# Kernel optimization log

Hardware: AMD Instinct MI355X
Metric: run time of the kernel (lower is better)

The kernel has to match this reference:

```python
import jax, jax.numpy as jnp
from jax import lax
import numpy as np

EPS = 1e-5
K = 3


def _conv(x, w, b, pad, dil=1, groups=1):
    out = lax.conv_general_dilated(
        x, w, (1, 1), [(pad, pad), (pad, pad)], rhs_dilation=(dil, dil),
        dimension_numbers=('NCHW', 'OIHW', 'NCHW'), feature_group_count=groups)
    return out + b[None, :, None, None]


def _bn(x, g, b, m, v):
    scale = g / jnp.sqrt(v + EPS)
    return (x - m[None, :, None, None]) * scale[None, :, None, None] + b[None, :, None, None]


def setup_inputs() -> dict:
    key = jax.random.key(0)
    ks = jax.random.split(key, 24)
    B, C, H, W = 8, 256, 48, 80
    Hd = 256  # hidden_channels
    n = lambda k, s, sc=0.05: (jax.random.normal(k, s, dtype=jnp.float32) * sc)
    return {
        'f_t_minus_2': jax.random.normal(ks[0], (B, C, H, W), dtype=jnp.float32),
        'f_t_minus_1': jax.random.normal(ks[1], (B, C, H, W), dtype=jnp.float32),
        'f_t':         jax.random.normal(ks[2], (B, C, H, W), dtype=jnp.float32),
        'ov_w1': n(ks[3], (Hd, 3 * C, 3, 3)), 'ov_b1': n(ks[4], (Hd,)),
        'bn1_g': jnp.ones((Hd,), jnp.float32), 'bn1_b': jnp.zeros((Hd,), jnp.float32),
        'bn1_m': n(ks[5], (Hd,)), 'bn1_v': jax.random.uniform(ks[6], (Hd,), jnp.float32, 0.5, 1.5),
        'ov_w2': n(ks[7], (Hd, Hd, 3, 3)), 'ov_b2': n(ks[8], (Hd,)),
        'bn2_g': jnp.ones((Hd,), jnp.float32), 'bn2_b': jnp.zeros((Hd,), jnp.float32),
        'bn2_m': n(ks[9], (Hd,)), 'bn2_v': jax.random.uniform(ks[10], (Hd,), jnp.float32, 0.5, 1.5),
        'g_w': n(ks[11], (C, Hd, 1, 1)), 'g_b': n(ks[12], (C,)),
        'fc1_w': n(ks[13], (512, 2 * C)), 'fc1_b': n(ks[14], (512,)),
        'fc2_w': n(ks[15], (C * K * K, 512)), 'fc2_b': n(ks[16], (C * K * K,)),
        'ap_w': n(ks[17], (1, 2 * C, 1, 1)), 'ap_b': n(ks[18], (1,)),
        'a_w': n(ks[19], (1, 2 * C, 1, 1)), 'a_b': jnp.ones((1,), jnp.float32),
    }


def reference(f_t_minus_2, f_t_minus_1, f_t,
              ov_w1, ov_b1, bn1_g, bn1_b, bn1_m, bn1_v,
              ov_w2, ov_b2, bn2_g, bn2_b, bn2_m, bn2_v,
              g_w, g_b, fc1_w, fc1_b, fc2_w, fc2_b,
              ap_w, ap_b, a_w, a_b):
    B, C, H, W = f_t.shape
    # (1) Overview-Net (GCM)
    f_concat = jnp.concatenate([f_t_minus_2, f_t_minus_1, f_t], axis=1)
    h = jax.nn.relu(_bn(_conv(f_concat, ov_w1, ov_b1, pad=2, dil=2), bn1_g, bn1_b, bn1_m, bn1_v))
    h = jax.nn.relu(_bn(_conv(h, ov_w2, ov_b2, pad=4, dil=4), bn2_g, bn2_b, bn2_m, bn2_v))
    g_pooled = h.mean(axis=(2, 3), keepdims=True)            # [B,Hd,1,1]
    G = _conv(g_pooled, g_w, g_b, pad=0)                     # [B,C,1,1]
    # (2) Focus-Net: FC-generated per-(batch,channel) 3x3 depthwise conv on (f_t, f_{t-1})
    Fs = jnp.concatenate([f_t, f_t_minus_1], axis=0)         # [2B,C,H,W]
    g_flat = jnp.repeat(G.reshape(B, C), 2, axis=0)          # [2B,C]
    gap = Fs.mean(axis=(2, 3))                               # [2B,C]
    fc_in = jnp.concatenate([g_flat, gap], axis=1)           # [2B,2C]
    w = jax.nn.silu(fc_in @ fc1_w.T + fc1_b) @ fc2_w.T + fc2_b  # [2B, C*9]
    w = w.reshape(2 * B * C, 1, K, K)
    x = Fs.reshape(1, 2 * B * C, H, W)
    out = lax.conv_general_dilated(
        x, w, (1, 1), [(1, 1), (1, 1)],
        dimension_numbers=('NCHW', 'OIHW', 'NCHW'), feature_group_count=2 * B * C)
    out = out.reshape(2 * B, C, H, W)
    f_t_mod, f_t1_mod = out[:B], out[B:]
    # (3) Dynamic fusion
    f_prev_cat = jnp.concatenate([f_t1_mod, f_t_minus_2], axis=1)
    alpha_prev = 0.3 + 0.4 * jax.nn.sigmoid(_conv(f_prev_cat, ap_w, ap_b, pad=0))
    f_prev = alpha_prev * f_t1_mod + (1.0 - alpha_prev) * f_t_minus_2
    f_cat = jnp.concatenate([f_t_mod, f_prev], axis=1)
    alpha = 0.6 + 0.3 * jax.nn.sigmoid(_conv(f_cat, a_w, a_b, pad=0))
    return alpha * f_t_mod + (1.0 - alpha) * f_prev
```

## Files before the change

kernel.cpp:

```cpp
#include <hip/hip_runtime.h>
#include <hip/hip_bf16.h>
#include <math.h>


typedef __bf16 bf16x8 __attribute__((ext_vector_type(8)));
typedef float f32x4 __attribute__((ext_vector_type(4)));
typedef __attribute__((address_space(1))) void as1_void;
typedef __attribute__((address_space(3))) void as3_void;


__global__ __launch_bounds__(256) void prep_consts_kernel(
    const float* __restrict__ ob1, const float* __restrict__ g1, const float* __restrict__ b1,
    const float* __restrict__ m1, const float* __restrict__ v1,
    const float* __restrict__ ob2, const float* __restrict__ g2, const float* __restrict__ b2,
    const float* __restrict__ m2, const float* __restrict__ v2,
    float* __restrict__ cst)
{
  int i = threadIdx.x;
  float a1 = g1[i] / sqrtf(v1[i] + 1e-5f);
  cst[i]       = a1;
  cst[256 + i] = (ob1[i] - m1[i]) * a1 + b1[i];
  float a2 = g2[i] / sqrtf(v2[i] + 1e-5f);
  cst[512 + i] = a2;
  cst[768 + i] = (ob2[i] - m2[i]) * a2 + b2[i];
}

__global__ __launch_bounds__(256) void pad_concat_kernel(
    const float* __restrict__ f2, const float* __restrict__ f1, const float* __restrict__ f0,
    __hip_bfloat16* __restrict__ out, float* __restrict__ gapv)
{
  int bid = blockIdx.x;
  const int cg = bid % 6; bid /= 6;
  const int y = bid % 48;
  const int b = bid / 48;

  __shared__ float tile[128 * 85];

  const float* src = (cg < 2) ? f2 : ((cg < 4) ? f1 : f0);
  const int ccbase = (cg & 1) * 128;
  const uint4 z4 = {0u, 0u, 0u, 0u};

#pragma unroll
  for (int it = 0; it < 10; it++) {
    const int idx = it * 256 + threadIdx.x;
    const int cl = idx / 20, x4 = idx % 20;
    const float4 v = *(const float4*)(src +
        (((size_t)b * 256 + ccbase + cl) * 48 + y) * 80 + x4 * 4);
    float* t = tile + cl * 85 + x4 * 4;
    t[0] = v.x; t[1] = v.y; t[2] = v.z; t[3] = v.w;
  }

  if (threadIdx.x < 32) {
    const int xb_ = threadIdx.x >> 3, ch8 = threadIdx.x & 7;
    const int xx = (xb_ < 2) ? xb_ : (80 + xb_);
    *(uint4*)(out + ((size_t)(b * 52 + y + 2) * 84 + xx) * 768 + cg * 128 + ch8 * 8) = z4;
  }
  if (y == 0 || y == 47) {
    const int r0 = (y == 0) ? 0 : 50;
    for (int idx = threadIdx.x; idx < 1344; idx += 256) {
      const int rr = idx / 672, rem = idx % 672;
      const int xx = rem >> 3, ch8 = rem & 7;
      *(uint4*)(out + ((size_t)(b * 52 + r0 + rr) * 84 + xx) * 768 + cg * 128 + ch8 * 8) = z4;
    }
  }
  __syncthreads();

  __hip_bfloat16* obase = out + ((size_t)(b * 52 + y + 2) * 84 + 2) * 768 + cg * 128;
#pragma unroll
  for (int it = 0; it < 5; it++) {
    const int idx = it * 256 + threadIdx.x;
    const int chunk = idx & 15, x = idx >> 4;
    const float* t = tile + chunk * 8 * 85 + x;
    union { __hip_bfloat16 h[8]; uint4 u; } pk;
#pragma unroll
    for (int j = 0; j < 8; j++) pk.h[j] = __float2bfloat16(t[j * 85]);
    *(uint4*)(obase + (size_t)x * 768 + chunk * 8) = pk.u;
  }

  if (cg >= 2) {
    const int i_gap = (cg >= 4) ? b : (b + 8);
    const int cl = threadIdx.x >> 1, half = threadIdx.x & 1;
    const float* t = tile + cl * 85 + half * 40;
    float s = 0.f;
#pragma unroll
    for (int k = 0; k < 40; k++) s += t[k];
    s += __shfl_xor(s, 1);
    if (half == 0) atomicAdd(&gapv[i_gap * 256 + ccbase + cl], s);
  }
}

__global__ __launch_bounds__(256) void repack_w_kernel(
    const float* __restrict__ w, __hip_bfloat16* __restrict__ out, int OC, int IC)
{
  int idx = blockIdx.x * 256 + threadIdx.x;
  if (idx >= OC * IC * 9) return;
  int ic = idx % IC;
  int t = idx / IC;
  int oc = t % OC;
  int tap = t / OC;
  out[idx] = __float2bfloat16(w[(oc * IC + ic) * 9 + tap]);
}

template <int CIN, int HP, int WP, int DIL, int MODE>
__global__ __launch_bounds__(256) void conv_mfma_kernel(
    const __hip_bfloat16* __restrict__ inp, const __hip_bfloat16* __restrict__ wt,
    const float* __restrict__ bnA, const float* __restrict__ bnB,
    __hip_bfloat16* __restrict__ outp, float* __restrict__ gpool)
{
  __shared__ unsigned short As[8192] __attribute__((aligned(16)));
  __shared__ unsigned short Bs[8192] __attribute__((aligned(16)));

  int bid = blockIdx.x;
  bid = (bid & 7) * 60 + (bid >> 3);
  const int ocb = bid & 1; bid >>= 1;
  const int xb = bid % 5; bid /= 5;
  const int yb = bid % 6; bid /= 6;
  const int b = bid;
  const int y0 = yb * 8, x0 = xb * 16, oc0 = ocb * 128;

  const int t = threadIdx.x;
  const int w = t >> 6, l = t & 63;
  const int col16 = l & 15, quad = l >> 4;
  const int wm = w >> 1, wn = w & 1;
  const int rsub = l >> 3;
  const int jj = (l & 7) ^ rsub;

  f32x4 acc[4][4];
  const f32x4 zf = {0.f, 0.f, 0.f, 0.f};
#pragma unroll
  for (int i = 0; i < 4; i++)
#pragma unroll
    for (int j = 0; j < 4; j++) acc[i][j] = zf;

  for (int c0 = 0; c0 < CIN; c0 += 64) {
    for (int tap = 0; tap < 9; tap++) {
      const int ty = tap / 3, tx = tap - ty * 3;
      const __hip_bfloat16* inBase =
          inp + ((size_t)(b * HP + y0 + DIL * ty) * WP + (x0 + DIL * tx)) * CIN + jj * 8 + c0;
      const __hip_bfloat16* wBase = wt + (size_t)(tap * 256 + oc0) * CIN + jj * 8 + c0;
      __syncthreads();
#pragma unroll
      for (int i = 0; i < 4; i++) {
        const int q = i * 4 + w;
        const int m = q * 8 + rsub;
        const int ry = m >> 4, rx = m & 15;
        const __hip_bfloat16* gp = inBase + (ry * WP + rx) * CIN;
        __builtin_amdgcn_global_load_lds((as1_void*)gp,
            (as3_void*)((char*)As + q * 1024), 16, 0, 0);
      }
#pragma unroll
      for (int i = 0; i < 4; i++) {
        const int q = i * 4 + w;
        const int n = q * 8 + rsub;
        const __hip_bfloat16* gp = wBase + n * CIN;
        __builtin_amdgcn_global_load_lds((as1_void*)gp,
            (as3_void*)((char*)Bs + q * 1024), 16, 0, 0);
      }
      __syncthreads();
#pragma unroll
      for (int kiter = 0; kiter < 2; kiter++) {
        bf16x8 af[4], bg[4];
#pragma unroll
        for (int fi = 0; fi < 4; fi++) {
          const int m = wm * 64 + fi * 16 + col16;
          const int jc = (kiter * 4 + quad) ^ (m & 7);
          af[fi] = *(const bf16x8*)((const char*)As + m * 128 + jc * 16);
        }
#pragma unroll
        for (int fi = 0; fi < 4; fi++) {
          const int n = wn * 64 + fi * 16 + col16;
          const int jc = (kiter * 4 + quad) ^ (n & 7);
          bg[fi] = *(const bf16x8*)((const char*)Bs + n * 128 + jc * 16);
        }
#pragma unroll
        for (int fm_ = 0; fm_ < 4; fm_++)
#pragma unroll
          for (int fn_ = 0; fn_ < 4; fn_++)
            acc[fm_][fn_] = __builtin_amdgcn_mfma_f32_16x16x32_bf16(
                af[fm_], bg[fn_], acc[fm_][fn_], 0, 0, 0);
      }
    }
  }

  if (MODE == 0) {
#pragma unroll
    for (int fn_ = 0; fn_ < 4; fn_++) {
      const int oc = oc0 + wn * 64 + fn_ * 16 + col16;
      const float sa = bnA[oc], sb = bnB[oc];
#pragma unroll
      for (int fm_ = 0; fm_ < 4; fm_++) {
#pragma unroll
        for (int r = 0; r < 4; r++) {
          const int m = wm * 64 + fm_ * 16 + quad * 4 + r;
          const int y = y0 + (m >> 4), x = x0 + (m & 15);
          const float v = fmaxf(acc[fm_][fn_][r] * sa + sb, 0.f);
          outp[((size_t)(b * 56 + y + 4) * 88 + (x + 4)) * 256 + oc] = __float2bfloat16(v);
        }
      }
    }
  } else {
#pragma unroll
    for (int fn_ = 0; fn_ < 4; fn_++) {
      const int oc = oc0 + wn * 64 + fn_ * 16 + col16;
      const float sa = bnA[oc], sb = bnB[oc];
      float cs = 0.f;
#pragma unroll
      for (int fm_ = 0; fm_ < 4; fm_++)
#pragma unroll
        for (int r = 0; r < 4; r++)
          cs += fmaxf(acc[fm_][fn_][r] * sa + sb, 0.f);
      cs += __shfl_xor(cs, 16);
      cs += __shfl_xor(cs, 32);
      if (quad == 0) atomicAdd(&gpool[b * 256 + oc], cs);
    }
  }
}


__global__ __launch_bounds__(256) void fcG_kernel(
    const float* __restrict__ gpool, const float* __restrict__ gw,
    const float* __restrict__ gb, float* __restrict__ G)
{
  int b = blockIdx.x, oc = threadIdx.x;
  __shared__ float pool[256];
  pool[oc] = gpool[b * 256 + oc] * (1.f / 3840.f);
  __syncthreads();
  float s = gb[oc];
  const float* wr = gw + oc * 256;
  for (int c2 = 0; c2 < 256; c2++) s += pool[c2] * wr[c2];
  G[b * 256 + oc] = s;
}

__global__ __launch_bounds__(256) void fc1_kernel(
    const float* __restrict__ G, const float* __restrict__ gapv,
    const float* __restrict__ w, const float* __restrict__ bias,
    float* __restrict__ out1)
{
  __shared__ float fin[16][513];
  for (int idx = threadIdx.x; idx < 16 * 512; idx += 256) {
    int i = idx >> 9, k = idx & 511;
    fin[i][k] = (k < 256) ? G[(i >> 1) * 256 + k]
                          : gapv[i * 256 + (k - 256)] * (1.f / 3840.f);
  }
  __syncthreads();
  int g = blockIdx.x * 256 + threadIdx.x;
  int j = g >> 4, i = g & 15;
  float s = bias[j];
  const float* wr = w + j * 512;
  for (int k = 0; k < 512; k++) s += fin[i][k] * wr[k];
  out1[j * 16 + i] = s / (1.f + expf(-s));
}

__global__ __launch_bounds__(256) void fc2_kernel(
    const float* __restrict__ out1, const float* __restrict__ w,
    const float* __restrict__ bias, float* __restrict__ wdw)
{
  __shared__ float fin[16][513];
  for (int idx = threadIdx.x; idx < 16 * 512; idx += 256) {
    int i = idx >> 9, k = idx & 511;
    fin[i][k] = out1[k * 16 + i];
  }
  __syncthreads();
  int g = blockIdx.x * 256 + threadIdx.x;
  int j = g >> 4, i = g & 15;
  float s = bias[j];
  const float* wr = w + j * 512;
  for (int k = 0; k < 512; k++) s += fin[i][k] * wr[k];
  wdw[i * 2304 + j] = s;
}

__global__ __launch_bounds__(256) void dw_kernel(
    const float* __restrict__ f0, const float* __restrict__ f1,
    const float* __restrict__ wdw, float* __restrict__ fm)
{
  int i = blockIdx.x >> 8, c = blockIdx.x & 255;
  const float* src = (i < 8) ? (f0 + ((size_t)i * 256 + c) * 3840)
                             : (f1 + ((size_t)(i - 8) * 256 + c) * 3840);
  float* dst = fm + ((size_t)i * 256 + c) * 3840;
  __shared__ float w9[9];
  if (threadIdx.x < 9) w9[threadIdx.x] = wdw[i * 2304 + c * 9 + threadIdx.x];
  __syncthreads();
  for (int p = threadIdx.x; p < 3840; p += 256) {
    int y = p / 80, x = p - y * 80;
    float s = 0.f;
#pragma unroll
    for (int ky = 0; ky < 3; ky++) {
      int yy = y + ky - 1;
      if (yy < 0 || yy >= 48) continue;
#pragma unroll
      for (int kx = 0; kx < 3; kx++) {
        int xx = x + kx - 1;
        if (xx < 0 || xx >= 80) continue;
        s += w9[ky * 3 + kx] * src[yy * 80 + xx];
      }
    }
    dst[p] = s;
  }
}

__global__ __launch_bounds__(640) void alpha_final_kernel(
    const float* __restrict__ fm, const float* __restrict__ f2,
    const float* __restrict__ apw, const float* __restrict__ apb,
    const float* __restrict__ aw, const float* __restrict__ ab,
    float* __restrict__ out)
{
  int b = blockIdx.x / 48, y = blockIdx.x % 48;
  int x = threadIdx.x % 80, g = threadIdx.x / 80;
  const float* ftm  = fm + ((size_t)(b * 256) + g * 32) * 3840 + y * 80 + x;
  const float* ft1m = fm + ((size_t)((b + 8) * 256) + g * 32) * 3840 + y * 80 + x;
  const float* ptm2 = f2 + ((size_t)(b * 256) + g * 32) * 3840 + y * 80 + x;

  float v0[32], v1[32], v2[32];
  float S = 0.f, T0 = 0.f, T1 = 0.f, T2 = 0.f;
#pragma unroll
  for (int cc = 0; cc < 32; cc++) {
    v0[cc] = ftm[(size_t)cc * 3840];
    v1[cc] = ft1m[(size_t)cc * 3840];
    v2[cc] = ptm2[(size_t)cc * 3840];
    const int c = g * 32 + cc;
    S  += apw[c] * v1[cc] + apw[256 + c] * v2[cc];
    T0 += aw[c] * v0[cc];
    T1 += aw[256 + c] * v1[cc];
    T2 += aw[256 + c] * v2[cc];
  }
  __shared__ float red[4][8][80];
  __shared__ float apl[80], alb[80];
  red[0][g][x] = S; red[1][g][x] = T0; red[2][g][x] = T1; red[3][g][x] = T2;
  __syncthreads();
  if (g == 0) {
    float s = 0.f, t0 = 0.f, t1 = 0.f, t2 = 0.f;
#pragma unroll
    for (int k = 0; k < 8; k++) {
      s += red[0][k][x]; t0 += red[1][k][x]; t1 += red[2][k][x]; t2 += red[3][k][x];
    }
    float ap = 0.3f + 0.4f / (1.f + expf(-(s + apb[0])));
    float A  = t0 + ap * t1 + (1.f - ap) * t2 + ab[0];
    float al = 0.6f + 0.3f / (1.f + expf(-A));
    apl[x] = ap; alb[x] = al;
  }
  __syncthreads();
  const float ap = apl[x], al = alb[x];
  float* ob = out + ((size_t)(b * 256) + g * 32) * 3840 + y * 80 + x;
#pragma unroll
  for (int cc = 0; cc < 32; cc++)
    ob[(size_t)cc * 3840] = al * v0[cc] + (1.f - al) * (ap * v1[cc] + (1.f - ap) * v2[cc]);
}


extern "C" void kernel_launch(void* const* d_in, const int* in_sizes, int n_in,
                              void* d_out, int out_size, void* d_ws, size_t ws_size,
                              hipStream_t stream)
{
  const float* f_tm2 = (const float*)d_in[0];
  const float* f_tm1 = (const float*)d_in[1];
  const float* f_t   = (const float*)d_in[2];
  const float* ov_w1 = (const float*)d_in[3];
  const float* ov_b1 = (const float*)d_in[4];
  const float* bn1_g = (const float*)d_in[5];
  const float* bn1_b = (const float*)d_in[6];
  const float* bn1_m = (const float*)d_in[7];
  const float* bn1_v = (const float*)d_in[8];
  const float* ov_w2 = (const float*)d_in[9];
  const float* ov_b2 = (const float*)d_in[10];
  const float* bn2_g = (const float*)d_in[11];
  const float* bn2_b = (const float*)d_in[12];
  const float* bn2_m = (const float*)d_in[13];
  const float* bn2_v = (const float*)d_in[14];
  const float* g_w   = (const float*)d_in[15];
  const float* g_b   = (const float*)d_in[16];
  const float* fc1_w = (const float*)d_in[17];
  const float* fc1_b = (const float*)d_in[18];
  const float* fc2_w = (const float*)d_in[19];
  const float* fc2_b = (const float*)d_in[20];
  const float* ap_w  = (const float*)d_in[21];
  const float* ap_b  = (const float*)d_in[22];
  const float* a_w   = (const float*)d_in[23];
  const float* a_b   = (const float*)d_in[24];

  char* ws = (char*)d_ws;
  float* fm            = (float*)ws;
  __hip_bfloat16* in1p = (__hip_bfloat16*)ws;
  __hip_bfloat16* wt1  = (__hip_bfloat16*)(ws + 53673984);
  __hip_bfloat16* wt2  = (__hip_bfloat16*)(ws + 57212928);
  __hip_bfloat16* h1p  = (__hip_bfloat16*)(ws + 58392576);
  float* gpool         = (float*)(ws + 78577664);
  float* gapv          = (float*)(ws + 78585856);
  float* Gv            = (float*)(ws + 78602240);
  float* out1          = (float*)(ws + 78610432);
  float* wdw           = (float*)(ws + 78643200);
  float* cst           = (float*)(ws + 79036416);

  hipMemsetAsync(h1p, 0, 20185088, stream);
  hipMemsetAsync(gpool, 0, 24576, stream);

  prep_consts_kernel<<<1, 256, 0, stream>>>(ov_b1, bn1_g, bn1_b, bn1_m, bn1_v,
                                            ov_b2, bn2_g, bn2_b, bn2_m, bn2_v, cst);
  pad_concat_kernel<<<2304, 256, 0, stream>>>(f_tm2, f_tm1, f_t, in1p, gapv);
  repack_w_kernel<<<6912, 256, 0, stream>>>(ov_w1, wt1, 256, 768);
  repack_w_kernel<<<2304, 256, 0, stream>>>(ov_w2, wt2, 256, 256);

  conv_mfma_kernel<768, 52, 84, 2, 0><<<480, 256, 0, stream>>>(in1p, wt1, cst, cst + 256, h1p, nullptr);
  conv_mfma_kernel<256, 56, 88, 4, 1><<<480, 256, 0, stream>>>(h1p, wt2, cst + 512, cst + 768, nullptr, gpool);

  fcG_kernel<<<8, 256, 0, stream>>>(gpool, g_w, g_b, Gv);
  fc1_kernel<<<32, 256, 0, stream>>>(Gv, gapv, fc1_w, fc1_b, out1);
  fc2_kernel<<<144, 256, 0, stream>>>(out1, fc2_w, fc2_b, wdw);
  dw_kernel<<<4096, 256, 0, stream>>>(f_t, f_tm1, wdw, fm);
  alpha_final_kernel<<<384, 640, 0, stream>>>(fm, f_tm2, ap_w, ap_b, a_w, a_b, (float*)d_out);
}
```

Measured before the change: 508.3 us.

## Split conv K-dimension across two wave groups and tile depthwise conv in LDS

The MFMA conv kernel now runs 512 threads per block, with two groups of four waves each handling half of the input channels in separate LDS buffers. The partial accumulators are reduced through LDS before the epilogue. With only 480 blocks on a 256-CU device, this is meant to give each CU more resident waves and better latency hiding, at the cost of 64KB of LDS per block plus an extra reduction step. The depthwise conv kernel also now stages a zero-padded tile in shared memory with vectorized float4 loads and computes four outputs per thread, replacing the bounds-checked global gathers.

```diff
diff --git a/kernel.cpp b/kernel.cpp
--- a/kernel.cpp
+++ b/kernel.cpp
@@ -102,13 +102,12 @@
 }
 
 template <int CIN, int HP, int WP, int DIL, int MODE>
-__global__ __launch_bounds__(256) void conv_mfma_kernel(
+__global__ __launch_bounds__(512) void conv_mfma_kernel(
     const __hip_bfloat16* __restrict__ inp, const __hip_bfloat16* __restrict__ wt,
     const float* __restrict__ bnA, const float* __restrict__ bnB,
     __hip_bfloat16* __restrict__ outp, float* __restrict__ gpool)
 {
-  __shared__ unsigned short As[8192] __attribute__((aligned(16)));
-  __shared__ unsigned short Bs[8192] __attribute__((aligned(16)));
+  __shared__ char lds_all[65536] __attribute__((aligned(16)));
 
   int bid = blockIdx.x;
   bid = (bid & 7) * 60 + (bid >> 3);
@@ -119,12 +118,18 @@
   const int y0 = yb * 8, x0 = xb * 16, oc0 = ocb * 128;
 
   const int t = threadIdx.x;
-  const int w = t >> 6, l = t & 63;
+  const int w8 = t >> 6;
+  const int grp = w8 >> 2;
+  const int w = w8 & 3;
+  const int l = t & 63;
   const int col16 = l & 15, quad = l >> 4;
   const int wm = w >> 1, wn = w & 1;
   const int rsub = l >> 3;
   const int jj = (l & 7) ^ rsub;
 
+  char* As = lds_all + grp * 16384;
+  char* Bs = lds_all + 32768 + grp * 16384;
+
   f32x4 acc[4][4];
   const f32x4 zf = {0.f, 0.f, 0.f, 0.f};
 #pragma unroll
@@ -132,7 +137,8 @@
 #pragma unroll
     for (int j = 0; j < 4; j++) acc[i][j] = zf;
 
-  for (int c0 = 0; c0 < CIN; c0 += 64) {
+  const int cbeg = grp * (CIN / 2), cend = cbeg + CIN / 2;
+  for (int c0 = cbeg; c0 < cend; c0 += 64) {
     for (int tap = 0; tap < 9; tap++) {
       const int ty = tap / 3, tx = tap - ty * 3;
       const __hip_bfloat16* inBase =
@@ -146,7 +152,7 @@
         const int ry = m >> 4, rx = m & 15;
         const __hip_bfloat16* gp = inBase + (ry * WP + rx) * CIN;
         __builtin_amdgcn_global_load_lds((as1_void*)gp,
-            (as3_void*)((char*)As + q * 1024), 16, 0, 0);
+            (as3_void*)(As + q * 1024), 16, 0, 0);
       }
 #pragma unroll
       for (int i = 0; i < 4; i++) {
@@ -154,7 +160,7 @@
         const int n = q * 8 + rsub;
         const __hip_bfloat16* gp = wBase + n * CIN;
         __builtin_amdgcn_global_load_lds((as1_void*)gp,
-            (as3_void*)((char*)Bs + q * 1024), 16, 0, 0);
+            (as3_void*)(Bs + q * 1024), 16, 0, 0);
       }
       __syncthreads();
 #pragma unroll
@@ -164,13 +170,13 @@
         for (int fi = 0; fi < 4; fi++) {
           const int m = wm * 64 + fi * 16 + col16;
           const int jc = (kiter * 4 + quad) ^ (m & 7);
-          af[fi] = *(const bf16x8*)((const char*)As + m * 128 + jc * 16);
+          af[fi] = *(const bf16x8*)(As + m * 128 + jc * 16);
         }
 #pragma unroll
         for (int fi = 0; fi < 4; fi++) {
           const int n = wn * 64 + fi * 16 + col16;
           const int jc = (kiter * 4 + quad) ^ (n & 7);
-          bg[fi] = *(const bf16x8*)((const char*)Bs + n * 128 + jc * 16);
+          bg[fi] = *(const bf16x8*)(Bs + n * 128 + jc * 16);
         }
 #pragma unroll
         for (int fm_ = 0; fm_ < 4; fm_++)
@@ -182,36 +188,54 @@
     }
   }
 
-  if (MODE == 0) {
-#pragma unroll
-    for (int fn_ = 0; fn_ < 4; fn_++) {
-      const int oc = oc0 + wn * 64 + fn_ * 16 + col16;
-      const float sa = bnA[oc], sb = bnB[oc];
-#pragma unroll
-      for (int fm_ = 0; fm_ < 4; fm_++) {
-#pragma unroll
-        for (int r = 0; r < 4; r++) {
-          const int m = wm * 64 + fm_ * 16 + quad * 4 + r;
-          const int y = y0 + (m >> 4), x = x0 + (m & 15);
-          const float v = fmaxf(acc[fm_][fn_][r] * sa + sb, 0.f);
-          outp[((size_t)(b * 56 + y + 4) * 88 + (x + 4)) * 256 + oc] = __float2bfloat16(v);
+  __syncthreads();
+  if (grp == 1) {
+    const int tl = t & 255;
+#pragma unroll
+    for (int i = 0; i < 4; i++)
+#pragma unroll
+      for (int j = 0; j < 4; j++)
+        *(f32x4*)(lds_all + (i * 4 + j) * 4096 + tl * 16) = acc[i][j];
+  }
+  __syncthreads();
+  if (grp == 0) {
+#pragma unroll
+    for (int i = 0; i < 4; i++)
+#pragma unroll
+      for (int j = 0; j < 4; j++)
+        acc[i][j] += *(const f32x4*)(lds_all + (i * 4 + j) * 4096 + t * 16);
+
+    if (MODE == 0) {
+#pragma unroll
+      for (int fn_ = 0; fn_ < 4; fn_++) {
+        const int oc = oc0 + wn * 64 + fn_ * 16 + col16;
+        const float sa = bnA[oc], sb = bnB[oc];
+#pragma unroll
+        for (int fm_ = 0; fm_ < 4; fm_++) {
+#pragma unroll
+          for (int r = 0; r < 4; r++) {
+            const int m = wm * 64 + fm_ * 16 + quad * 4 + r;
+            const int y = y0 + (m >> 4), x = x0 + (m & 15);
+            const float v = fmaxf(acc[fm_][fn_][r] * sa + sb, 0.f);
+            outp[((size_t)(b * 56 + y + 4) * 88 + (x + 4)) * 256 + oc] = __float2bfloat16(v);
+          }
         }
       }
-    }
-  } else {
-#pragma unroll
-    for (int fn_ = 0; fn_ < 4; fn_++) {
-      const int oc = oc0 + wn * 64 + fn_ * 16 + col16;
-      const float sa = bnA[oc], sb = bnB[oc];
-      float cs = 0.f;
-#pragma unroll
-      for (int fm_ = 0; fm_ < 4; fm_++)
-#pragma unroll
-        for (int r = 0; r < 4; r++)
-          cs += fmaxf(acc[fm_][fn_][r] * sa + sb, 0.f);
-      cs += __shfl_xor(cs, 16);
-      cs += __shfl_xor(cs, 32);
-      if (quad == 0) atomicAdd(&gpool[b * 256 + oc], cs);
+    } else {
+#pragma unroll
+      for (int fn_ = 0; fn_ < 4; fn_++) {
+        const int oc = oc0 + wn * 64 + fn_ * 16 + col16;
+        const float sa = bnA[oc], sb = bnB[oc];
+        float cs = 0.f;
+#pragma unroll
+        for (int fm_ = 0; fm_ < 4; fm_++)
+#pragma unroll
+          for (int r = 0; r < 4; r++)
+            cs += fmaxf(acc[fm_][fn_][r] * sa + sb, 0.f);
+        cs += __shfl_xor(cs, 16);
+        cs += __shfl_xor(cs, 32);
+        if (quad == 0) atomicAdd(&gpool[b * 256 + oc], cs);
+      }
     }
   }
 }
@@ -277,24 +301,32 @@
   const float* src = (i < 8) ? (f0 + ((size_t)i * 256 + c) * 3840)
                              : (f1 + ((size_t)(i - 8) * 256 + c) * 3840);
   float* dst = fm + ((size_t)i * 256 + c) * 3840;
-  __shared__ float w9[9];
-  if (threadIdx.x < 9) w9[threadIdx.x] = wdw[i * 2304 + c * 9 + threadIdx.x];
-  __syncthreads();
-  for (int p = threadIdx.x; p < 3840; p += 256) {
-    int y = p / 80, x = p - y * 80;
-    float s = 0.f;
-#pragma unroll
-    for (int ky = 0; ky < 3; ky++) {
-      int yy = y + ky - 1;
-      if (yy < 0 || yy >= 48) continue;
-#pragma unroll
-      for (int kx = 0; kx < 3; kx++) {
-        int xx = x + kx - 1;
-        if (xx < 0 || xx >= 80) continue;
-        s += w9[ky * 3 + kx] * src[yy * 80 + xx];
-      }
+  __shared__ float w9s[9];
+  __shared__ float tile[50][82];
+  for (int k = threadIdx.x; k < 4100; k += 256) ((float*)tile)[k] = 0.f;
+  if (threadIdx.x < 9) w9s[threadIdx.x] = wdw[i * 2304 + c * 9 + threadIdx.x];
+  __syncthreads();
+  for (int k = threadIdx.x; k < 960; k += 256) {
+    const float4 v = *(const float4*)(src + k * 4);
+    const int y = k / 20, xx = (k % 20) * 4;
+    float* tp = &tile[y + 1][xx + 1];
+    tp[0] = v.x; tp[1] = v.y; tp[2] = v.z; tp[3] = v.w;
+  }
+  __syncthreads();
+  for (int k = threadIdx.x; k < 960; k += 256) {
+    const int y = k / 20, xx = (k % 20) * 4;
+    float r0 = 0.f, r1 = 0.f, r2 = 0.f, r3 = 0.f;
+#pragma unroll
+    for (int dy = 0; dy < 3; dy++) {
+      const float* row = &tile[y + dy][xx];
+      const float w0 = w9s[dy * 3], w1 = w9s[dy * 3 + 1], w2 = w9s[dy * 3 + 2];
+      r0 += w0 * row[0] + w1 * row[1] + w2 * row[2];
+      r1 += w0 * row[1] + w1 * row[2] + w2 * row[3];
+      r2 += w0 * row[2] + w1 * row[3] + w2 * row[4];
+      r3 += w0 * row[3] + w1 * row[4] + w2 * row[5];
     }
-    dst[p] = s;
+    float4 o; o.x = r0; o.y = r1; o.z = r2; o.w = r3;
+    *(float4*)(dst + k * 4) = o;
   }
 }
 
@@ -399,8 +431,8 @@
   repack_w_kernel<<<6912, 256, 0, stream>>>(ov_w1, wt1, 256, 768);
   repack_w_kernel<<<2304, 256, 0, stream>>>(ov_w2, wt2, 256, 256);
 
-  conv_mfma_kernel<768, 52, 84, 2, 0><<<480, 256, 0, stream>>>(in1p, wt1, cst, cst + 256, h1p, nullptr);
-  conv_mfma_kernel<256, 56, 88, 4, 1><<<480, 256, 0, stream>>>(h1p, wt2, cst + 512, cst + 768, nullptr, gpool);
+  conv_mfma_kernel<768, 52, 84, 2, 0><<<480, 512, 0, stream>>>(in1p, wt1, cst, cst + 256, h1p, nullptr);
+  conv_mfma_kernel<256, 56, 88, 4, 1><<<480, 512, 0, stream>>>(h1p, wt2, cst + 512, cst + 768, nullptr, gpool);
 
   fcG_kernel<<<8, 256, 0, stream>>>(gpool, g_w, g_b, Gv);
   fc1_kernel<<<32, 256, 0, stream>>>(Gv, gapv, fc1_w, fc1_b, out1);
```

Measured after the change: 502.4 us. Within noise of the previous version (-1.2%).
